# Performance work log

Hardware: AMD Instinct MI355X
Metric: run time of the kernel (lower is better)

The kernel has to match this reference:

```python
import jax, jax.numpy as jnp
import numpy as np

HEADS = 8
NEG = -1e9
EPS = 1e-9


def setup_inputs() -> dict:
    key = jax.random.key(0)
    ks = jax.random.split(key, 24)
    N, D, E = 2048, 512, 64
    s = 0.02
    inp = {
        "xyz": jax.random.normal(ks[0], (N, 3), jnp.float32),
        "str_feat": jax.random.normal(ks[1], (N, D), jnp.float32),
        "esm_feat": jax.random.normal(ks[2], (N, E), jnp.float32),
        "y_hat": jax.random.uniform(ks[3], (N, 1), jnp.float32),
        "distance_mask": jax.random.randint(ks[4], (N, N), 0, 2, jnp.int32),
        "t": jnp.ones((1,), jnp.float32),
        "band_width": jnp.ones((1,), jnp.float32),
        "max_iter": 5,
        # main projections (torch Linear layout: y = x @ W.T + b)
        "Wq": jax.random.normal(ks[5], (D, D), jnp.float32) * s,
        "bq": jnp.zeros((D,), jnp.float32),
        "Wk": jax.random.normal(ks[6], (D, D), jnp.float32) * s,
        "bk": jnp.zeros((D,), jnp.float32),
        "Wv": jax.random.normal(ks[7], (D, D), jnp.float32) * s,
        "bv": jnp.zeros((D,), jnp.float32),
        "Wo": jax.random.normal(ks[8], (D, D), jnp.float32) * s,
        "bo": jnp.zeros((D,), jnp.float32),
        # esm projections (computed in the original forward but unused downstream)
        "Weq": jax.random.normal(ks[9], (E, E), jnp.float32) * s,
        "beq": jnp.zeros((E,), jnp.float32),
        "Wek": jax.random.normal(ks[10], (E, E), jnp.float32) * s,
        "bek": jnp.zeros((E,), jnp.float32),
        "Wev": jax.random.normal(ks[11], (E, E), jnp.float32) * s,
        "bev": jnp.zeros((E,), jnp.float32),
        "Weo": jax.random.normal(ks[12], (E, E), jnp.float32) * s,
        "beo": jnp.zeros((E,), jnp.float32),
    }
    return inp


def reference(xyz, str_feat, esm_feat, y_hat, distance_mask, t, band_width, max_iter,
              Wq, bq, Wk, bk, Wv, bv, Wo, bo,
              Weq, beq, Wek, bek, Wev, bev, Weo, beo):
    N, D = str_feat.shape
    h = HEADS
    dh = D // h

    q = str_feat @ Wq.T + bq
    k = str_feat @ Wk.T + bk
    v = str_feat @ Wv.T + bv
    # esm projections: computed in the original forward but never used (dead code; DCE'd under jit)
    _esm_q = esm_feat @ Weq.T + beq
    _esm_k = esm_feat @ Wek.T + bek
    _esm_v = esm_feat @ Wev.T + bev

    # [h, N, dh]
    qh = q.reshape(N, h, dh).transpose(1, 0, 2)
    kh = k.reshape(N, h, dh).transpose(1, 0, 2)
    vh = v.reshape(N, h, dh).transpose(1, 0, 2)

    scores = jnp.einsum('hnd,hmd->hnm', qh, kh) / jnp.sqrt(jnp.asarray(dh, qh.dtype))
    mask = (distance_mask > 0)[None]              # [1, N, N]
    yw = y_hat[:, 0][None, :]                     # [1, N] per-target weight
    inv_two_bw2 = 1.0 / (2.0 * band_width[0] ** 2)
    temp = t[0]

    def step(carry, _):
        xyz_c, _x = carry
        # squared pairwise distances via the expanded form (avoids [N,N,3])
        sq = jnp.sum(xyz_c * xyz_c, axis=-1)
        d2 = sq[:, None] + sq[None, :] - 2.0 * (xyz_c @ xyz_c.T)
        kern = jnp.exp(-d2 * inv_two_bw2)          # [N, N] band-width kernel
        logits = scores / temp + jnp.log(kern * yw + EPS)[None]
        logits = jnp.where(mask, logits, NEG)
        attn = jax.nn.softmax(logits, axis=-1)     # [h, N, N]
        xyz_new = jnp.einsum('nm,md->nd', attn.mean(0), xyz_c)  # mean-shift step
        x_new = jnp.einsum('hnm,hmd->hnd', attn, vh)            # [h, N, dh]
        return (xyz_new, x_new), None

    (xyz_out, xh), _ = jax.lax.scan(step, (xyz, jnp.zeros_like(vh)), None, length=max_iter)
    x = xh.transpose(1, 0, 2).reshape(N, D)
    out = x @ Wo.T + bo
    return xyz_out, out
```

## Files before the change

### kernel.cpp

```cpp
#include <hip/hip_runtime.h>


typedef __attribute__((ext_vector_type(8))) short bf16x8;
typedef __attribute__((ext_vector_type(4))) float f32x4;

__device__ __forceinline__ unsigned short f2bf(float f) {
    unsigned int u = __float_as_uint(f);
    u += 0x7fff + ((u >> 16) & 1);
    return (unsigned short)(u >> 16);
}
__device__ __forceinline__ float bf2f(unsigned short u) {
    return __uint_as_float((unsigned int)u << 16);
}

union EU { bf16x8 v; unsigned short u[8]; };

__global__ __launch_bounds__(256)
void conv_all(const float* __restrict__ strf,
              const float* __restrict__ Wq, const float* __restrict__ Wk,
              const float* __restrict__ Wv, const float* __restrict__ Wo,
              const int* __restrict__ dmask,
              unsigned short* __restrict__ sA, unsigned short* __restrict__ sW,
              unsigned char* __restrict__ mby)
{
    const long base = (long)(blockIdx.x * 256 + threadIdx.x) * 8;
    if (base >= 2097152) {
        const long rel = base - 2097152;
        int4 a = *reinterpret_cast<const int4*>(dmask + rel);
        int4 b = *reinterpret_cast<const int4*>(dmask + rel + 4);
        unsigned long long p = 0;
        p |= (a.x > 0) ? 0x01ULL : 0;  p |= (a.y > 0) ? 0x0100ULL : 0;
        p |= (a.z > 0) ? 0x010000ULL : 0;  p |= (a.w > 0) ? 0x01000000ULL : 0;
        p |= (b.x > 0) ? 0x0100000000ULL : 0;  p |= (b.y > 0) ? 0x010000000000ULL : 0;
        p |= (b.z > 0) ? 0x01000000000000ULL : 0;  p |= (b.w > 0) ? 0x0100000000000000ULL : 0;
        *reinterpret_cast<unsigned long long*>(mby + rel) = p;
        return;
    }
    const float* src;
    unsigned short* dst;
    if (base < 1048576) {
        src = strf + base; dst = sA + base;
    } else {
        const long rel = base - 1048576;
        const int seg = (int)(rel >> 18);
        const long off = rel & 262143;
        const float* Ws[4] = {Wq, Wk, Wv, Wo};
        src = Ws[seg] + off;
        dst = sW + (long)seg * 262144 + off;
    }
    float4 a = *reinterpret_cast<const float4*>(src);
    float4 b = *reinterpret_cast<const float4*>(src + 4);
    EU o;
    o.u[0] = f2bf(a.x); o.u[1] = f2bf(a.y); o.u[2] = f2bf(a.z); o.u[3] = f2bf(a.w);
    o.u[4] = f2bf(b.x); o.u[5] = f2bf(b.y); o.u[6] = f2bf(b.z); o.u[7] = f2bf(b.w);
    *reinterpret_cast<bf16x8*>(dst) = o.v;
}

__global__ __launch_bounds__(256)
void qkv_mfma(const unsigned short* __restrict__ sA,
              const unsigned short* __restrict__ sW,
              const float* __restrict__ bq, const float* __restrict__ bk,
              const float* __restrict__ bv,
              unsigned short* __restrict__ qh, unsigned short* __restrict__ kh,
              unsigned short* __restrict__ vT)
{
    const int z  = blockIdx.z;
    const int bx = blockIdx.x;
    const int by = blockIdx.y;
    const int tid = threadIdx.x;
    const int wv = tid >> 6;
    const int lane = tid & 63;
    const int row  = lane & 15;
    const int koct = (lane >> 4) * 8;
    const int n0 = bx * 64;

    const unsigned short* Ap = sA + (long)(n0 + wv * 16 + row) * 512;
    const unsigned short* Bp = sW + (long)z * 262144 + (long)(by * 64 + row) * 512;

    f32x4 acc[4] = {};
#pragma unroll
    for (int k0 = 0; k0 < 512; k0 += 32) {
        bf16x8 a = *reinterpret_cast<const bf16x8*>(Ap + k0 + koct);
#pragma unroll
        for (int t = 0; t < 4; t++) {
            bf16x8 b = *reinterpret_cast<const bf16x8*>(Bp + (long)(t * 16) * 512 + k0 + koct);
            acc[t] = __builtin_amdgcn_mfma_f32_16x16x32_bf16(a, b, acc[t], 0, 0, 0);
        }
    }

    if (z == 2) {
        const int rbase = n0 + wv * 16 + (lane >> 4) * 4;
#pragma unroll
        for (int t = 0; t < 4; t++) {
            const int d = by * 64 + t * 16 + (lane & 15);
            const float bb = bv[d];
            ushort4 o;
            o.x = f2bf(acc[t][0] + bb); o.y = f2bf(acc[t][1] + bb);
            o.z = f2bf(acc[t][2] + bb); o.w = f2bf(acc[t][3] + bb);
            *reinterpret_cast<ushort4*>(vT + (long)d * 2048 + rbase) = o;
        }
        return;
    }

    __shared__ float ls[64][68];
    const int lrb = wv * 16 + (lane >> 4) * 4;
    const int lcb = lane & 15;
#pragma unroll
    for (int t = 0; t < 4; t++)
#pragma unroll
        for (int r = 0; r < 4; r++)
            ls[lrb + r][t * 16 + lcb] = acc[t][r];
    __syncthreads();

    const float* bias = (z == 0) ? bq : bk;
    unsigned short* dst = (z == 0) ? qh : kh;
    const int r2 = tid >> 2;
    const int c2 = (tid & 3) * 16;
    float sv[16];
#pragma unroll
    for (int j = 0; j < 4; j++) {
        float4 s = *reinterpret_cast<const float4*>(&ls[r2][c2 + j * 4]);
        float4 bb = *reinterpret_cast<const float4*>(bias + by * 64 + c2 + j * 4);
        sv[j*4+0] = s.x + bb.x; sv[j*4+1] = s.y + bb.y;
        sv[j*4+2] = s.z + bb.z; sv[j*4+3] = s.w + bb.w;
    }
    EU o0, o1;
#pragma unroll
    for (int j = 0; j < 8; j++) { o0.u[j] = f2bf(sv[j]); o1.u[j] = f2bf(sv[8 + j]); }
    unsigned short* dp = dst + (long)(n0 + r2) * 512 + by * 64 + c2;
    *reinterpret_cast<bf16x8*>(dp)     = o0.v;
    *reinterpret_cast<bf16x8*>(dp + 8) = o1.v;
}

__global__ __launch_bounds__(256)
void scores_rows(const unsigned short* __restrict__ qh,
                 const unsigned short* __restrict__ kh,
                 const unsigned char* __restrict__ mby,
                 const float* __restrict__ tptr,
                 unsigned short* __restrict__ Ebf)
{
    const int h  = blockIdx.y;
    const int n0 = blockIdx.x * 16;
    const int tid = threadIdx.x;
    const int wv = tid >> 6;
    const int lane = tid & 63;
    const float scale = 1.0f / (8.0f * tptr[0]);

    __shared__ unsigned short lsb[4][16][268];

    const int arow = lane & 15;
    const int koct = (lane >> 4) * 8;
    const unsigned short* Aq = qh + (long)(n0 + arow) * 512 + h * 64;
    const bf16x8 aq0 = *reinterpret_cast<const bf16x8*>(Aq + koct);
    const bf16x8 aq1 = *reinterpret_cast<const bf16x8*>(Aq + 32 + koct);

    const int lr = (lane >> 4) * 4;
    const int lc = lane & 15;
    const int rrd = lane & 15;
    const int cgr = (lane >> 4) * 64;

#pragma unroll
    for (int half = 0; half < 2; half++) {
        const int mbase = wv * 512 + half * 256;
#pragma unroll
        for (int mt = 0; mt < 16; mt++) {
            const int m0 = mbase + mt * 16;
            const unsigned short* Bk = kh + (long)(m0 + arow) * 512 + h * 64;
            bf16x8 b0 = *reinterpret_cast<const bf16x8*>(Bk + koct);
            bf16x8 b1 = *reinterpret_cast<const bf16x8*>(Bk + 32 + koct);
            f32x4 c = {};
            c = __builtin_amdgcn_mfma_f32_16x16x32_bf16(aq0, b0, c, 0, 0, 0);
            c = __builtin_amdgcn_mfma_f32_16x16x32_bf16(aq1, b1, c, 0, 0, 0);
#pragma unroll
            for (int r = 0; r < 4; r++)
                lsb[wv][lr + r][mt * 16 + lc] = f2bf(__expf(c[r] * scale));
        }
        const int gn = n0 + rrd;
        const int mabs = mbase + cgr;
        const unsigned char* mp = mby + (long)gn * 2048 + mabs;
        unsigned short* ep = Ebf + ((long)h * 2048 + gn) * 2048 + mabs;
#pragma unroll
        for (int c8 = 0; c8 < 8; c8++) {
            EU e;
            e.v = *reinterpret_cast<const bf16x8*>(&lsb[wv][rrd][cgr + c8 * 8]);
            unsigned long long mk = *reinterpret_cast<const unsigned long long*>(mp + c8 * 8);
            EU o;
#pragma unroll
            for (int j = 0; j < 8; j++)
                o.u[j] = ((mk >> (8 * j)) & 0xff) ? e.u[j] : (unsigned short)0;
            *reinterpret_cast<bf16x8*>(ep + c8 * 8) = o.v;
        }
    }
}

__global__ __launch_bounds__(256)
void ms_iter(const unsigned short* __restrict__ Ebf,
             const float* __restrict__ xyz_src,
             float* __restrict__ xyz_dst,
             const float* __restrict__ y_hat,
             const float* __restrict__ bwp,
             unsigned short* __restrict__ attn_out,
             int write_attn)
{
    const int n = blockIdx.x;
    const int tid = threadIdx.x;
    const int lane = tid & 63;
    const int wave = tid >> 6;
    const int m0 = tid * 8;

    __shared__ float red[64];

    EU E[8];
#pragma unroll
    for (int h = 0; h < 8; h++)
        E[h].v = *reinterpret_cast<const bf16x8*>(Ebf + (long)h * 4194304 + (long)n * 2048 + m0);

    const float bw = bwp[0];
    const float c2k = 1.0f / (2.0f * bw * bw);

    const float xn = xyz_src[n * 3 + 0];
    const float yn = xyz_src[n * 3 + 1];
    const float zn = xyz_src[n * 3 + 2];
    const float sqn = xn * xn + yn * yn + zn * zn;

    float mx[8], my[8], mz[8];
    {
        const float4* xp = reinterpret_cast<const float4*>(xyz_src + (long)m0 * 3);
        float4 a = xp[0], b = xp[1], c = xp[2], d = xp[3], e = xp[4], f = xp[5];
        mx[0]=a.x; my[0]=a.y; mz[0]=a.z;  mx[1]=a.w; my[1]=b.x; mz[1]=b.y;
        mx[2]=b.z; my[2]=b.w; mz[2]=c.x;  mx[3]=c.y; my[3]=c.z; mz[3]=c.w;
        mx[4]=d.x; my[4]=d.y; mz[4]=d.z;  mx[5]=d.w; my[5]=e.x; mz[5]=e.y;
        mx[6]=e.z; my[6]=e.w; mz[6]=f.x;  mx[7]=f.y; my[7]=f.z; mz[7]=f.w;
    }
    float4 yh0 = *reinterpret_cast<const float4*>(y_hat + m0);
    float4 yh1 = *reinterpret_cast<const float4*>(y_hat + m0 + 4);
    float yh[8] = {yh0.x, yh0.y, yh0.z, yh0.w, yh1.x, yh1.y, yh1.z, yh1.w};

    float g[8];
#pragma unroll
    for (int j = 0; j < 8; j++) {
        const float d2 = sqn + (mx[j]*mx[j] + my[j]*my[j] + mz[j]*mz[j])
                       - 2.0f * (xn*mx[j] + yn*my[j] + zn*mz[j]);
        g[j] = __expf(-d2 * c2k) * yh[j] + 1e-9f;
    }

    float z[8];
#pragma unroll
    for (int h = 0; h < 8; h++) {
        float zz = 0.f;
#pragma unroll
        for (int j = 0; j < 8; j++) zz += bf2f(E[h].u[j]) * g[j];
        z[h] = zz;
    }

#pragma unroll
    for (int h = 0; h < 8; h++) {
        float v = z[h];
#pragma unroll
        for (int off = 32; off > 0; off >>= 1) v += __shfl_down(v, off, 64);
        if (lane == 0) red[wave * 8 + h] = v;
    }
    __syncthreads();
    if (tid < 8) {
        const float s = red[tid] + red[8 + tid] + red[16 + tid] + red[24 + tid];
        red[32 + tid] = 1.0f / s;
    }
    __syncthreads();
    float invz[8];
#pragma unroll
    for (int h = 0; h < 8; h++) invz[h] = red[32 + h];
    __syncthreads();

    float ax = 0.f, ay = 0.f, az = 0.f;
#pragma unroll
    for (int j = 0; j < 8; j++) {
        float w = 0.f;
#pragma unroll
        for (int h = 0; h < 8; h++) w += bf2f(E[h].u[j]) * invz[h];
        w *= 0.125f * g[j];
        ax += w * mx[j]; ay += w * my[j]; az += w * mz[j];
    }
    if (write_attn) {
#pragma unroll
        for (int h = 0; h < 8; h++) {
            EU o;
#pragma unroll
            for (int j = 0; j < 8; j++)
                o.u[j] = f2bf(bf2f(E[h].u[j]) * g[j] * invz[h]);
            *reinterpret_cast<bf16x8*>(attn_out + (long)h * 4194304 + (long)n * 2048 + m0) = o.v;
        }
    }

    float v3[3] = {ax, ay, az};
#pragma unroll
    for (int c = 0; c < 3; c++) {
        float v = v3[c];
#pragma unroll
        for (int off = 32; off > 0; off >>= 1) v += __shfl_down(v, off, 64);
        if (lane == 0) red[c * 4 + wave] = v;
    }
    __syncthreads();
    if (tid < 3) {
        xyz_dst[n * 3 + tid] = red[tid * 4 + 0] + red[tid * 4 + 1] +
                               red[tid * 4 + 2] + red[tid * 4 + 3];
    }
}

__global__ __launch_bounds__(256)
void av_mfma(const unsigned short* __restrict__ attn,
             const unsigned short* __restrict__ vT,
             float* __restrict__ P)
{
    const int h  = blockIdx.z;
    const int s  = blockIdx.y;
    const int bx = blockIdx.x;
    const int wv = threadIdx.x >> 6;
    const int lane = threadIdx.x & 63;
    const int n0 = bx * 64 + wv * 16;
    const int kc = s * 512;

    const int mrow = lane & 15;
    const int koct = (lane >> 4) * 8;

    const unsigned short* Ab = attn + (long)h * 4194304 + (long)(n0 + mrow) * 2048;
    const unsigned short* Bb = vT + ((long)h * 64 + mrow) * 2048;

    f32x4 acc[4] = {};
    for (int k0 = kc; k0 < kc + 512; k0 += 32) {
        bf16x8 a = *reinterpret_cast<const bf16x8*>(Ab + k0 + koct);
#pragma unroll
        for (int t = 0; t < 4; t++) {
            bf16x8 b = *reinterpret_cast<const bf16x8*>(Bb + (long)(t * 16) * 2048 + k0 + koct);
            acc[t] = __builtin_amdgcn_mfma_f32_16x16x32_bf16(a, b, acc[t], 0, 0, 0);
        }
    }

    float* Pp = P + (long)s * 1048576;
    const int rbase = n0 + (lane >> 4) * 4;
    const int dcol = lane & 15;
#pragma unroll
    for (int t = 0; t < 4; t++)
#pragma unroll
        for (int r = 0; r < 4; r++)
            Pp[(long)(rbase + r) * 512 + h * 64 + t * 16 + dcol] = acc[t][r];
}

__global__ __launch_bounds__(256)
void av_red(const float* __restrict__ P, unsigned short* __restrict__ xc)
{
    const long idx = (long)(blockIdx.x * 256 + threadIdx.x) * 8;
    float s[8] = {};
#pragma unroll
    for (int p = 0; p < 4; p++) {
        const float* pp = P + (long)p * 1048576 + idx;
        float4 a = *reinterpret_cast<const float4*>(pp);
        float4 b = *reinterpret_cast<const float4*>(pp + 4);
        s[0] += a.x; s[1] += a.y; s[2] += a.z; s[3] += a.w;
        s[4] += b.x; s[5] += b.y; s[6] += b.z; s[7] += b.w;
    }
    EU o;
#pragma unroll
    for (int j = 0; j < 8; j++) o.u[j] = f2bf(s[j]);
    *reinterpret_cast<bf16x8*>(xc + idx) = o.v;
}

__global__ __launch_bounds__(256)
void out_mfma(const unsigned short* __restrict__ xc,
              const unsigned short* __restrict__ sW,
              const float* __restrict__ bo,
              float* __restrict__ out)
{
    const int bx = blockIdx.x;
    const int by = blockIdx.y;
    const int wv = threadIdx.x >> 6;
    const int lane = threadIdx.x & 63;
    const int row  = lane & 15;
    const int koct = (lane >> 4) * 8;
    const int n0 = bx * 64;

    const unsigned short* Ap = xc + (long)(n0 + wv * 16 + row) * 512;
    const unsigned short* Bp = sW + 3L * 262144 + (long)(by * 64 + row) * 512;

    f32x4 acc[4] = {};
#pragma unroll
    for (int k0 = 0; k0 < 512; k0 += 32) {
        bf16x8 a = *reinterpret_cast<const bf16x8*>(Ap + k0 + koct);
#pragma unroll
        for (int t = 0; t < 4; t++) {
            bf16x8 b = *reinterpret_cast<const bf16x8*>(Bp + (long)(t * 16) * 512 + k0 + koct);
            acc[t] = __builtin_amdgcn_mfma_f32_16x16x32_bf16(a, b, acc[t], 0, 0, 0);
        }
    }

    const int rbase = n0 + wv * 16 + (lane >> 4) * 4;
    const int dcol = lane & 15;
#pragma unroll
    for (int t = 0; t < 4; t++) {
        const int col = by * 64 + t * 16 + dcol;
        const float bb = bo[col];
#pragma unroll
        for (int r = 0; r < 4; r++)
            out[(long)(rbase + r) * 512 + col] = acc[t][r] + bb;
    }
}

extern "C" void kernel_launch(void* const* d_in, const int* in_sizes, int n_in,
                              void* d_out, int out_size, void* d_ws, size_t ws_size,
                              hipStream_t stream)
{
    (void)in_sizes; (void)n_in; (void)out_size; (void)ws_size;

    const float* xyz   = (const float*)d_in[0];
    const float* strf  = (const float*)d_in[1];
    const float* yhat  = (const float*)d_in[3];
    const int*   dmask = (const int*)d_in[4];
    const float* tptr  = (const float*)d_in[5];
    const float* bwptr = (const float*)d_in[6];
    const float* Wq = (const float*)d_in[8];
    const float* bq = (const float*)d_in[9];
    const float* Wk = (const float*)d_in[10];
    const float* bk = (const float*)d_in[11];
    const float* Wv = (const float*)d_in[12];
    const float* bv = (const float*)d_in[13];
    const float* Wo = (const float*)d_in[14];
    const float* bo = (const float*)d_in[15];
    float* outp = (float*)d_out;

    char* wsb = (char*)d_ws;
    float* Ppart         = (float*)(wsb);
    unsigned short* xc   = (unsigned short*)(wsb + (16L << 20));
    unsigned short* sA   = (unsigned short*)(wsb + (18L << 20));
    unsigned short* sW   = (unsigned short*)(wsb + (20L << 20));
    unsigned short* qh   = (unsigned short*)(wsb + (22L << 20));
    unsigned short* kh   = (unsigned short*)(wsb + (24L << 20));
    unsigned short* vT   = (unsigned short*)(wsb + (26L << 20));
    float* xyzA          = (float*)(wsb + (28L << 20));
    float* xyzB          = xyzA + 8192;
    unsigned char* mby   = (unsigned char*)(wsb + (30L << 20));
    unsigned short* Ebf  = (unsigned short*)(wsb + (34L << 20));

    dim3 blk(256, 1, 1);

    conv_all<<<dim3(3072), blk, 0, stream>>>(strf, Wq, Wk, Wv, Wo, dmask, sA, sW, mby);
    qkv_mfma<<<dim3(32, 8, 3), blk, 0, stream>>>(sA, sW, bq, bk, bv, qh, kh, vT);

    scores_rows<<<dim3(128, 8), blk, 0, stream>>>(qh, kh, mby, tptr, Ebf);

    const float* src = xyz;
    float* dsts[5] = {xyzA, xyzB, xyzA, xyzB, outp};
    for (int it = 0; it < 5; it++) {
        ms_iter<<<dim3(2048), blk, 0, stream>>>(Ebf, src, dsts[it], yhat, bwptr,
                                                Ebf, it == 4 ? 1 : 0);
        src = dsts[it];
    }

    av_mfma<<<dim3(32, 4, 8), blk, 0, stream>>>(Ebf, vT, Ppart);
    av_red<<<dim3(512), blk, 0, stream>>>(Ppart, xc);
    out_mfma<<<dim3(32, 8), blk, 0, stream>>>(xc, sW, bo, outp + 6144);
}
```

Measured before the change: 368.3 us.

## Defer attention normalization into AV kernel and coalesce scores writeback

The final mean-shift iteration no longer writes the full normalized bf16 attention tensor for all heads. It stores only the per-row kernel weights g (shared across heads) and the per-head inverse normalizers, and the AV kernel rebuilds the attention tile in LDS from E, g and invz before the MFMA. This removes a full 8xNxN bf16 write and re-read pass, but adds extra reads of g, LDS staging and block barriers in av_mfma. The scores kernel's masked writeback is also remapped so each wave stores contiguous row segments, with a narrower LDS row pad.

```diff
diff --git a/kernel.cpp b/kernel.cpp
--- a/kernel.cpp
+++ b/kernel.cpp
@@ -146,7 +146,7 @@
     const int lane = tid & 63;
     const float scale = 1.0f / (8.0f * tptr[0]);
 
-    __shared__ unsigned short lsb[4][16][268];
+    __shared__ unsigned short lsb[4][16][260];
 
     const int arow = lane & 15;
     const int koct = (lane >> 4) * 8;
@@ -156,16 +156,15 @@
 
     const int lr = (lane >> 4) * 4;
     const int lc = lane & 15;
-    const int rrd = lane & 15;
-    const int cgr = (lane >> 4) * 64;
+    const int rlo = lane >> 5;
+    const int cch = lane & 31;
 
 #pragma unroll
     for (int half = 0; half < 2; half++) {
         const int mbase = wv * 512 + half * 256;
 #pragma unroll
         for (int mt = 0; mt < 16; mt++) {
-            const int m0 = mbase + mt * 16;
-            const unsigned short* Bk = kh + (long)(m0 + arow) * 512 + h * 64;
+            const unsigned short* Bk = kh + (long)(mbase + mt * 16 + arow) * 512 + h * 64;
             bf16x8 b0 = *reinterpret_cast<const bf16x8*>(Bk + koct);
             bf16x8 b1 = *reinterpret_cast<const bf16x8*>(Bk + 32 + koct);
             f32x4 c = {};
@@ -175,20 +174,20 @@
             for (int r = 0; r < 4; r++)
                 lsb[wv][lr + r][mt * 16 + lc] = f2bf(__expf(c[r] * scale));
         }
-        const int gn = n0 + rrd;
-        const int mabs = mbase + cgr;
-        const unsigned char* mp = mby + (long)gn * 2048 + mabs;
-        unsigned short* ep = Ebf + ((long)h * 2048 + gn) * 2048 + mabs;
-#pragma unroll
-        for (int c8 = 0; c8 < 8; c8++) {
+#pragma unroll
+        for (int rp = 0; rp < 8; rp++) {
+            const int row = rp * 2 + rlo;
+            const int gn = n0 + row;
+            const int m = mbase + cch * 8;
             EU e;
-            e.v = *reinterpret_cast<const bf16x8*>(&lsb[wv][rrd][cgr + c8 * 8]);
-            unsigned long long mk = *reinterpret_cast<const unsigned long long*>(mp + c8 * 8);
+            e.v = *reinterpret_cast<const bf16x8*>(&lsb[wv][row][cch * 8]);
+            unsigned long long mk =
+                *reinterpret_cast<const unsigned long long*>(mby + (long)gn * 2048 + m);
             EU o;
 #pragma unroll
             for (int j = 0; j < 8; j++)
                 o.u[j] = ((mk >> (8 * j)) & 0xff) ? e.u[j] : (unsigned short)0;
-            *reinterpret_cast<bf16x8*>(ep + c8 * 8) = o.v;
+            *reinterpret_cast<bf16x8*>(Ebf + ((long)h * 2048 + gn) * 2048 + m) = o.v;
         }
     }
 }
@@ -199,8 +198,9 @@
              float* __restrict__ xyz_dst,
              const float* __restrict__ y_hat,
              const float* __restrict__ bwp,
-             unsigned short* __restrict__ attn_out,
-             int write_attn)
+             unsigned short* __restrict__ gbf,
+             float* __restrict__ invzb,
+             int wlast)
 {
     const int n = blockIdx.x;
     const int tid = threadIdx.x;
@@ -263,7 +263,9 @@
     __syncthreads();
     if (tid < 8) {
         const float s = red[tid] + red[8 + tid] + red[16 + tid] + red[24 + tid];
-        red[32 + tid] = 1.0f / s;
+        const float iz = 1.0f / s;
+        red[32 + tid] = iz;
+        if (wlast) invzb[tid * 2048 + n] = iz;
     }
     __syncthreads();
     float invz[8];
@@ -280,15 +282,11 @@
         w *= 0.125f * g[j];
         ax += w * mx[j]; ay += w * my[j]; az += w * mz[j];
     }
-    if (write_attn) {
-#pragma unroll
-        for (int h = 0; h < 8; h++) {
-            EU o;
-#pragma unroll
-            for (int j = 0; j < 8; j++)
-                o.u[j] = f2bf(bf2f(E[h].u[j]) * g[j] * invz[h]);
-            *reinterpret_cast<bf16x8*>(attn_out + (long)h * 4194304 + (long)n * 2048 + m0) = o.v;
-        }
+    if (wlast) {
+        EU og;
+#pragma unroll
+        for (int j = 0; j < 8; j++) og.u[j] = f2bf(g[j]);
+        *reinterpret_cast<bf16x8*>(gbf + (long)n * 2048 + m0) = og.v;
     }
 
     float v3[3] = {ax, ay, az};
@@ -307,36 +305,60 @@
 }
 
 __global__ __launch_bounds__(256)
-void av_mfma(const unsigned short* __restrict__ attn,
+void av_mfma(const unsigned short* __restrict__ Ebf,
+             const unsigned short* __restrict__ gbf,
+             const float* __restrict__ invzb,
              const unsigned short* __restrict__ vT,
              float* __restrict__ P)
 {
     const int h  = blockIdx.z;
     const int s  = blockIdx.y;
     const int bx = blockIdx.x;
-    const int wv = threadIdx.x >> 6;
-    const int lane = threadIdx.x & 63;
-    const int n0 = bx * 64 + wv * 16;
+    const int tid = threadIdx.x;
+    const int wv = tid >> 6;
+    const int lane = tid & 63;
+    const int n0 = bx * 64;
     const int kc = s * 512;
+
+    __shared__ unsigned short As[64][132];
 
     const int mrow = lane & 15;
     const int koct = (lane >> 4) * 8;
-
-    const unsigned short* Ab = attn + (long)h * 4194304 + (long)(n0 + mrow) * 2048;
-    const unsigned short* Bb = vT + ((long)h * 64 + mrow) * 2048;
+    const int srow = tid >> 4;
+    const int skk  = (tid & 15) * 8;
 
     f32x4 acc[4] = {};
-    for (int k0 = kc; k0 < kc + 512; k0 += 32) {
-        bf16x8 a = *reinterpret_cast<const bf16x8*>(Ab + k0 + koct);
-#pragma unroll
-        for (int t = 0; t < 4; t++) {
-            bf16x8 b = *reinterpret_cast<const bf16x8*>(Bb + (long)(t * 16) * 2048 + k0 + koct);
-            acc[t] = __builtin_amdgcn_mfma_f32_16x16x32_bf16(a, b, acc[t], 0, 0, 0);
+    for (int kt = 0; kt < 4; kt++) {
+        const int kb = kc + kt * 128;
+        __syncthreads();
+#pragma unroll
+        for (int l = 0; l < 4; l++) {
+            const int row = l * 16 + srow;
+            EU e, gg;
+            e.v  = *reinterpret_cast<const bf16x8*>(Ebf + ((long)h * 2048 + n0 + row) * 2048 + kb + skk);
+            gg.v = *reinterpret_cast<const bf16x8*>(gbf + (long)(n0 + row) * 2048 + kb + skk);
+            const float iz = invzb[h * 2048 + n0 + row];
+            EU a;
+#pragma unroll
+            for (int j = 0; j < 8; j++)
+                a.u[j] = f2bf(bf2f(e.u[j]) * bf2f(gg.u[j]) * iz);
+            *reinterpret_cast<bf16x8*>(&As[row][skk]) = a.v;
+        }
+        __syncthreads();
+#pragma unroll
+        for (int k2 = 0; k2 < 128; k2 += 32) {
+            bf16x8 a = *reinterpret_cast<const bf16x8*>(&As[wv * 16 + mrow][k2 + koct]);
+#pragma unroll
+            for (int t = 0; t < 4; t++) {
+                bf16x8 b = *reinterpret_cast<const bf16x8*>(
+                    vT + ((long)h * 64 + t * 16 + mrow) * 2048 + kb + k2 + koct);
+                acc[t] = __builtin_amdgcn_mfma_f32_16x16x32_bf16(a, b, acc[t], 0, 0, 0);
+            }
         }
     }
 
     float* Pp = P + (long)s * 1048576;
-    const int rbase = n0 + (lane >> 4) * 4;
+    const int rbase = n0 + wv * 16 + (lane >> 4) * 4;
     const int dcol = lane & 15;
 #pragma unroll
     for (int t = 0; t < 4; t++)
@@ -438,6 +460,8 @@
     float* xyzB          = xyzA + 8192;
     unsigned char* mby   = (unsigned char*)(wsb + (30L << 20));
     unsigned short* Ebf  = (unsigned short*)(wsb + (34L << 20));
+    unsigned short* gbf  = (unsigned short*)(wsb + (98L << 20));
+    float* invzb         = (float*)(wsb + (106L << 20));
 
     dim3 blk(256, 1, 1);
 
@@ -450,11 +474,11 @@
     float* dsts[5] = {xyzA, xyzB, xyzA, xyzB, outp};
     for (int it = 0; it < 5; it++) {
         ms_iter<<<dim3(2048), blk, 0, stream>>>(Ebf, src, dsts[it], yhat, bwptr,
-                                                Ebf, it == 4 ? 1 : 0);
+                                                gbf, invzb, it == 4 ? 1 : 0);
         src = dsts[it];
     }
 
-    av_mfma<<<dim3(32, 4, 8), blk, 0, stream>>>(Ebf, vT, Ppart);
+    av_mfma<<<dim3(32, 4, 8), blk, 0, stream>>>(Ebf, gbf, invzb, vT, Ppart);
     av_red<<<dim3(512), blk, 0, stream>>>(Ppart, xc);
     out_mfma<<<dim3(32, 8), blk, 0, stream>>>(xc, sW, bo, outp + 6144);
 }
```

Result: faster. 321.8 us (-12.6%).

## Coalesce masked score stores and defer softmax normalization to AV reduction

Applied to the files above, without the earlier changes.

The scores kernel's LDS-to-global writeback is remapped so each pair of half-waves writes a full contiguous row segment, giving coalesced mask loads and E stores, and the LDS row padding is changed. The last mean-shift iteration now stores unnormalized attention numerators plus per-head 1/Z values. The 1/Z scale is applied in the AV partial-sum reduction instead of per element, which saves multiplies. This changes the rounding point of bf16 values (unnormalized values are rounded before scaling), and the new 260-element padding may introduce LDS bank conflicts.

```diff
diff --git a/kernel.cpp b/kernel.cpp
--- a/kernel.cpp
+++ b/kernel.cpp
@@ -146,7 +146,7 @@
     const int lane = tid & 63;
     const float scale = 1.0f / (8.0f * tptr[0]);
 
-    __shared__ unsigned short lsb[4][16][268];
+    __shared__ unsigned short lsb[4][16][260];
 
     const int arow = lane & 15;
     const int koct = (lane >> 4) * 8;
@@ -156,16 +156,15 @@
 
     const int lr = (lane >> 4) * 4;
     const int lc = lane & 15;
-    const int rrd = lane & 15;
-    const int cgr = (lane >> 4) * 64;
+    const int rlo = lane >> 5;
+    const int cch = lane & 31;
 
 #pragma unroll
     for (int half = 0; half < 2; half++) {
         const int mbase = wv * 512 + half * 256;
 #pragma unroll
         for (int mt = 0; mt < 16; mt++) {
-            const int m0 = mbase + mt * 16;
-            const unsigned short* Bk = kh + (long)(m0 + arow) * 512 + h * 64;
+            const unsigned short* Bk = kh + (long)(mbase + mt * 16 + arow) * 512 + h * 64;
             bf16x8 b0 = *reinterpret_cast<const bf16x8*>(Bk + koct);
             bf16x8 b1 = *reinterpret_cast<const bf16x8*>(Bk + 32 + koct);
             f32x4 c = {};
@@ -175,20 +174,20 @@
             for (int r = 0; r < 4; r++)
                 lsb[wv][lr + r][mt * 16 + lc] = f2bf(__expf(c[r] * scale));
         }
-        const int gn = n0 + rrd;
-        const int mabs = mbase + cgr;
-        const unsigned char* mp = mby + (long)gn * 2048 + mabs;
-        unsigned short* ep = Ebf + ((long)h * 2048 + gn) * 2048 + mabs;
-#pragma unroll
-        for (int c8 = 0; c8 < 8; c8++) {
+#pragma unroll
+        for (int rp = 0; rp < 8; rp++) {
+            const int row = rp * 2 + rlo;
+            const int gn = n0 + row;
+            const int m = mbase + cch * 8;
             EU e;
-            e.v = *reinterpret_cast<const bf16x8*>(&lsb[wv][rrd][cgr + c8 * 8]);
-            unsigned long long mk = *reinterpret_cast<const unsigned long long*>(mp + c8 * 8);
+            e.v = *reinterpret_cast<const bf16x8*>(&lsb[wv][row][cch * 8]);
+            unsigned long long mk =
+                *reinterpret_cast<const unsigned long long*>(mby + (long)gn * 2048 + m);
             EU o;
 #pragma unroll
             for (int j = 0; j < 8; j++)
                 o.u[j] = ((mk >> (8 * j)) & 0xff) ? e.u[j] : (unsigned short)0;
-            *reinterpret_cast<bf16x8*>(ep + c8 * 8) = o.v;
+            *reinterpret_cast<bf16x8*>(Ebf + ((long)h * 2048 + gn) * 2048 + m) = o.v;
         }
     }
 }
@@ -199,8 +198,9 @@
              float* __restrict__ xyz_dst,
              const float* __restrict__ y_hat,
              const float* __restrict__ bwp,
-             unsigned short* __restrict__ attn_out,
-             int write_attn)
+             unsigned short* __restrict__ Eout,
+             float* __restrict__ invzb,
+             int wlast)
 {
     const int n = blockIdx.x;
     const int tid = threadIdx.x;
@@ -263,7 +263,9 @@
     __syncthreads();
     if (tid < 8) {
         const float s = red[tid] + red[8 + tid] + red[16 + tid] + red[24 + tid];
-        red[32 + tid] = 1.0f / s;
+        const float iz = 1.0f / s;
+        red[32 + tid] = iz;
+        if (wlast) invzb[tid * 2048 + n] = iz;
     }
     __syncthreads();
     float invz[8];
@@ -280,14 +282,14 @@
         w *= 0.125f * g[j];
         ax += w * mx[j]; ay += w * my[j]; az += w * mz[j];
     }
-    if (write_attn) {
+    if (wlast) {
 #pragma unroll
         for (int h = 0; h < 8; h++) {
             EU o;
 #pragma unroll
             for (int j = 0; j < 8; j++)
-                o.u[j] = f2bf(bf2f(E[h].u[j]) * g[j] * invz[h]);
-            *reinterpret_cast<bf16x8*>(attn_out + (long)h * 4194304 + (long)n * 2048 + m0) = o.v;
+                o.u[j] = f2bf(bf2f(E[h].u[j]) * g[j]);
+            *reinterpret_cast<bf16x8*>(Eout + (long)h * 4194304 + (long)n * 2048 + m0) = o.v;
         }
     }
 
@@ -307,7 +309,7 @@
 }
 
 __global__ __launch_bounds__(256)
-void av_mfma(const unsigned short* __restrict__ attn,
+void av_mfma(const unsigned short* __restrict__ Eg,
              const unsigned short* __restrict__ vT,
              float* __restrict__ P)
 {
@@ -322,7 +324,7 @@
     const int mrow = lane & 15;
     const int koct = (lane >> 4) * 8;
 
-    const unsigned short* Ab = attn + (long)h * 4194304 + (long)(n0 + mrow) * 2048;
+    const unsigned short* Ab = Eg + ((long)h * 2048 + n0 + mrow) * 2048;
     const unsigned short* Bb = vT + ((long)h * 64 + mrow) * 2048;
 
     f32x4 acc[4] = {};
@@ -346,9 +348,13 @@
 }
 
 __global__ __launch_bounds__(256)
-void av_red(const float* __restrict__ P, unsigned short* __restrict__ xc)
+void av_red(const float* __restrict__ P, const float* __restrict__ invzb,
+            unsigned short* __restrict__ xc)
 {
     const long idx = (long)(blockIdx.x * 256 + threadIdx.x) * 8;
+    const int n = (int)(idx >> 9);
+    const int d0 = (int)(idx & 511);
+    const float iz = invzb[(d0 >> 6) * 2048 + n];
     float s[8] = {};
 #pragma unroll
     for (int p = 0; p < 4; p++) {
@@ -360,7 +366,7 @@
     }
     EU o;
 #pragma unroll
-    for (int j = 0; j < 8; j++) o.u[j] = f2bf(s[j]);
+    for (int j = 0; j < 8; j++) o.u[j] = f2bf(s[j] * iz);
     *reinterpret_cast<bf16x8*>(xc + idx) = o.v;
 }
 
@@ -438,6 +444,7 @@
     float* xyzB          = xyzA + 8192;
     unsigned char* mby   = (unsigned char*)(wsb + (30L << 20));
     unsigned short* Ebf  = (unsigned short*)(wsb + (34L << 20));
+    float* invzb         = (float*)(wsb + (98L << 20));
 
     dim3 blk(256, 1, 1);
 
@@ -450,11 +457,11 @@
     float* dsts[5] = {xyzA, xyzB, xyzA, xyzB, outp};
     for (int it = 0; it < 5; it++) {
         ms_iter<<<dim3(2048), blk, 0, stream>>>(Ebf, src, dsts[it], yhat, bwptr,
-                                                Ebf, it == 4 ? 1 : 0);
+                                                Ebf, invzb, it == 4 ? 1 : 0);
         src = dsts[it];
     }
 
     av_mfma<<<dim3(32, 4, 8), blk, 0, stream>>>(Ebf, vT, Ppart);
-    av_red<<<dim3(512), blk, 0, stream>>>(Ppart, xc);
+    av_red<<<dim3(512), blk, 0, stream>>>(Ppart, invzb, xc);
     out_mfma<<<dim3(32, 8), blk, 0, stream>>>(xc, sW, bo, outp + 6144);
 }
```

Result: faster. 352.9 us (-4.2%).
